# Kernel optimization log

Hardware: AMD Instinct MI355X
Metric: run time of the kernel (lower is better)

Reference implementation:

```python
import jax, jax.numpy as jnp
import numpy as np

DIM = 512
NUM_HEADS = 8
HEAD_DIM = DIM // NUM_HEADS
SCALE = HEAD_DIM ** -0.5
B, T = 8, 1024


def setup_inputs() -> dict:
    key = jax.random.key(0)
    ks = jax.random.split(key, 6)
    x = jax.random.normal(ks[0], (B, T, DIM), dtype=jnp.float32)
    attn_mask = jax.random.randint(ks[1], (B, T, T), 0, 2) == 1  # bool [B,T,T]
    s = 1.0 / np.sqrt(DIM)
    qkv_w = jax.random.uniform(ks[2], (3 * DIM, DIM), jnp.float32, -s, s)
    qkv_b = jax.random.uniform(ks[3], (3 * DIM,), jnp.float32, -s, s)
    proj_w = jax.random.uniform(ks[4], (DIM, DIM), jnp.float32, -s, s)
    proj_b = jax.random.uniform(ks[5], (DIM,), jnp.float32, -s, s)
    return {"x": x, "attn_mask": attn_mask, "qkv_w": qkv_w, "qkv_b": qkv_b,
            "proj_w": proj_w, "proj_b": proj_b}


def reference(x, attn_mask, qkv_w, qkv_b, proj_w, proj_b):
    b, t, c = x.shape
    # QKV projection (torch Linear: x @ W.T + b), split into q,k,v heads
    qkv = x @ qkv_w.T + qkv_b                      # [b,t,3*c]
    qkv = qkv.reshape(b, t, 3, NUM_HEADS, HEAD_DIM)
    qkv = jnp.transpose(qkv, (2, 0, 3, 1, 4))      # [3,b,h,t,d]
    q, k, v = qkv[0], qkv[1], qkv[2]
    scores = jnp.einsum('bhqd,bhkd->bhqk', q, k) * SCALE  # [b,h,t,t]
    min_val = jnp.finfo(scores.dtype).min
    scores = jnp.where(attn_mask[:, None, :, :], min_val, scores)
    attn = jax.nn.softmax(scores, axis=-1)
    out = jnp.einsum('bhqk,bhkd->bhqd', attn, v)   # [b,h,t,d]
    out = jnp.transpose(out, (0, 2, 1, 3)).reshape(b, t, c)
    return out @ proj_w.T + proj_b
```

## Files before the change

kernel.cpp:

```cpp
#include <hip/hip_runtime.h>
#include <math.h>

#define DIM   512
#define NH    8
#define HD    64
#define BATCH 8
#define SEQ   1024
#define QSCALE 0.18033688011112042f

typedef unsigned short u16;
typedef unsigned int   u32;
typedef unsigned long long u64;
typedef __bf16 bf16x8 __attribute__((ext_vector_type(8)));
typedef float  f32x4  __attribute__((ext_vector_type(4)));

__device__ inline u16 f2bf(float f) {
  u32 u = __builtin_bit_cast(u32, f);
  return (u16)((u + 0x7fffu + ((u >> 16) & 1u)) >> 16);
}
__device__ inline float bf2f(u16 h) {
  return __builtin_bit_cast(float, (u32)h << 16);
}
__device__ inline u32 pk2(float a, float b) {
  return (u32)f2bf(a) | ((u32)f2bf(b) << 16);
}

__device__ inline void a16(const u16* g, u16* l) {
  __builtin_amdgcn_global_load_lds(
      (const __attribute__((address_space(1))) u32*)g,
      (__attribute__((address_space(3))) u32*)l, 16, 0, 0);
}


__device__ inline void decomp_body(const float* __restrict__ src, u16* ph,
                                   u16* pl, int t) {
  #pragma unroll
  for (int c = 0; c < 4; ++c) {
    const int cid = c * 256 + t;
    const int row = cid & 15, kc = cid >> 4;
    float f[8];
    *(float4*)&f[0] = *(const float4*)&src[row * DIM + kc * 8];
    *(float4*)&f[4] = *(const float4*)&src[row * DIM + kc * 8 + 4];
    u16 hv[8], lv[8];
    #pragma unroll
    for (int j = 0; j < 8; ++j) {
      hv[j] = f2bf(f[j]);
      lv[j] = f2bf(f[j] - bf2f(hv[j]));
    }
    *(uint4*)&ph[(size_t)cid * 8] = *(const uint4*)hv;
    *(uint4*)&pl[(size_t)cid * 8] = *(const uint4*)lv;
  }
}

__global__ __launch_bounds__(256) void prep(
    const int* __restrict__ mask, u64* __restrict__ bits,
    const float* __restrict__ x, u16* __restrict__ xhi, u16* __restrict__ xlo,
    const float* __restrict__ qkvw, u16* __restrict__ wqh, u16* __restrict__ wql,
    const float* __restrict__ projw, u16* __restrict__ wph, u16* __restrict__ wpl) {
  const int blk = blockIdx.x;
  const int t = threadIdx.x;
  if (blk < 32768) {
    const size_t gid = (size_t)blk * 256 + t;
    const int lane = t & 63;
    const size_t w = gid >> 6;
    const int v = mask[w * 64 + lane];
    const u64 b = __ballot(v != 0);
    if (lane == 0) {
      const int bb = (int)(w >> 14), q = (int)((w >> 4) & 1023),
                kt = (int)(w & 15);
      bits[(((size_t)(bb << 4 | kt)) << 10) | q] = b;
    }
  } else if (blk < 33280) {
    const int rg = blk - 32768;
    decomp_body(x + (size_t)rg * 16 * DIM, xhi + (size_t)rg * 8192,
                xlo + (size_t)rg * 8192, t);
  } else if (blk < 33376) {
    const int rg = blk - 33280;
    decomp_body(qkvw + (size_t)rg * 16 * DIM, wqh + (size_t)rg * 8192,
                wql + (size_t)rg * 8192, t);
  } else {
    const int rg = blk - 33376;
    decomp_body(projw + (size_t)rg * 16 * DIM, wph + (size_t)rg * 8192,
                wpl + (size_t)rg * 8192, t);
  }
}

template <int MT, int NT, int WMT, int WNT, bool QKV>
__global__ __launch_bounds__(256) void mfma_gemm(
    const u16* __restrict__ Agh, const u16* __restrict__ Agl,
    const u16* __restrict__ Bgh, const u16* __restrict__ Bgl,
    const float* __restrict__ bias, void* __restrict__ out0,
    u16* __restrict__ kfr, u16* __restrict__ vfr) {
  __shared__ u16 sAh[MT * 512];
  __shared__ u16 sAl[MT * 512];
  __shared__ u16 sBh[NT * 512];
  __shared__ u16 sBl[NT * 512];

  const int tid = threadIdx.x;
  const int lane = tid & 63;
  const int wv = tid >> 6;
  const int lk = lane & 15, lq = lane >> 4;
  const int n0 = blockIdx.x * (NT * 16), m0 = blockIdx.y * (MT * 16);
  const int wm = (wv & 1) * WMT;
  const int wn = (wv >> 1) * WNT;

  const u16* gAh = Agh + (size_t)(m0 >> 4) * 8192 + lane * 8;
  const u16* gAl = Agl + (size_t)(m0 >> 4) * 8192 + lane * 8;
  const u16* gBh = Bgh + (size_t)(n0 >> 4) * 8192 + lane * 8;
  const u16* gBl = Bgl + (size_t)(n0 >> 4) * 8192 + lane * 8;

  f32x4 acc[WMT][WNT];
  #pragma unroll
  for (int i = 0; i < WMT; ++i)
    #pragma unroll
    for (int j = 0; j < WNT; ++j) acc[i][j] = (f32x4){0.f, 0.f, 0.f, 0.f};

  #pragma unroll 1
  for (int ki = 0; ki < 16; ++ki) {
    __syncthreads();
    if constexpr (MT == NT) {
      #pragma unroll
      for (int it = 0; it < MT / 4; ++it) {
        const int t = it * 4 + wv;
        const size_t go = (size_t)t * 8192 + ki * 512;
        const int lo_ = t * 512 + lane * 8;
        a16(gAh + go, &sAh[lo_]);
        a16(gAl + go, &sAl[lo_]);
        a16(gBh + go, &sBh[lo_]);
        a16(gBl + go, &sBl[lo_]);
      }
    } else {
      #pragma unroll
      for (int it = 0; it < MT / 4; ++it) {
        const int t = it * 4 + wv;
        const size_t go = (size_t)t * 8192 + ki * 512;
        const int lo_ = t * 512 + lane * 8;
        a16(gAh + go, &sAh[lo_]);
        a16(gAl + go, &sAl[lo_]);
      }
      #pragma unroll
      for (int it = 0; it < NT / 4; ++it) {
        const int t = it * 4 + wv;
        const size_t go = (size_t)t * 8192 + ki * 512;
        const int lo_ = t * 512 + lane * 8;
        a16(gBh + go, &sBh[lo_]);
        a16(gBl + go, &sBl[lo_]);
      }
    }
    __syncthreads();

    bf16x8 ah[WMT], al[WMT], bh[WNT], bl[WNT];
    #pragma unroll
    for (int i = 0; i < WMT; ++i) {
      ah[i] = *(const bf16x8*)&sAh[(wm + i) * 512 + lane * 8];
      al[i] = *(const bf16x8*)&sAl[(wm + i) * 512 + lane * 8];
    }
    #pragma unroll
    for (int j = 0; j < WNT; ++j) {
      bh[j] = *(const bf16x8*)&sBh[(wn + j) * 512 + lane * 8];
      bl[j] = *(const bf16x8*)&sBl[(wn + j) * 512 + lane * 8];
    }
    #pragma unroll
    for (int i = 0; i < WMT; ++i)
      #pragma unroll
      for (int j = 0; j < WNT; ++j) {
        acc[i][j] = __builtin_amdgcn_mfma_f32_16x16x32_bf16(ah[i], bh[j], acc[i][j], 0, 0, 0);
        acc[i][j] = __builtin_amdgcn_mfma_f32_16x16x32_bf16(ah[i], bl[j], acc[i][j], 0, 0, 0);
        acc[i][j] = __builtin_amdgcn_mfma_f32_16x16x32_bf16(al[i], bh[j], acc[i][j], 0, 0, 0);
      }
  }

  #pragma unroll
  for (int j = 0; j < WNT; ++j) {
    const int n = n0 + (wn + j) * 16 + lk;
    const float bv_ = bias[n];
    #pragma unroll
    for (int i = 0; i < WMT; ++i) {
      const int mb = m0 + (wm + i) * 16 + lq * 4;
      if (QKV) {
        const int which = n >> 9, h = (n >> 6) & 7, d = n & 63;
        const int b = mb >> 10, tok0 = mb & 1023;
        const size_t hb = (size_t)((b << 3) + h) << 16;
        if (which == 2) {
          const size_t base = hb + ((size_t)(tok0 >> 6) << 12) +
                              ((size_t)((d >> 4) & 3) << 10) +
                              ((size_t)((tok0 >> 5) & 1) << 9) +
                              ((size_t)((d & 15) + (((tok0 >> 3) & 3) << 4)) << 3) +
                              (size_t)(tok0 & 7);
          uint2 o2;
          o2.x = pk2(acc[i][j][0] + bv_, acc[i][j][1] + bv_);
          o2.y = pk2(acc[i][j][2] + bv_, acc[i][j][3] + bv_);
          *(uint2*)&vfr[base] = o2;
        } else if (which == 1) {
          const size_t base = hb + ((size_t)(tok0 >> 4) << 10) +
                              ((size_t)(d >> 5) << 9) + (size_t)(d & 7) +
                              ((size_t)(((d >> 3) & 3) << 4) << 3);
          #pragma unroll
          for (int r = 0; r < 4; ++r)
            kfr[base + (((tok0 & 15) + r) << 3)] = f2bf(acc[i][j][r] + bv_);
        } else {
          u16* dst = (u16*)out0;
          #pragma unroll
          for (int r = 0; r < 4; ++r)
            dst[(((size_t)((b << 3) + h) << 10 | (tok0 + r)) << 6) + d] =
                f2bf((acc[i][j][r] + bv_) * QSCALE);
        }
      } else {
        #pragma unroll
        for (int r = 0; r < 4; ++r)
          ((float*)out0)[(size_t)(mb + r) * DIM + n] = acc[i][j][r] + bv_;
      }
    }
  }
}

__global__ __launch_bounds__(256) void attn_mfma(
    const u16* __restrict__ qg, const u16* __restrict__ kfr,
    const u16* __restrict__ vfr, const u64* __restrict__ bitsT,
    u16* __restrict__ ohi, u16* __restrict__ olo) {
  __shared__ u16 Kls[4096];
  __shared__ u16 Vls[4096];
  __shared__ u16 Ps[64 * 72];

  const int tid = threadIdx.x;
  const int lane = tid & 63;
  const int wv = tid >> 6;
  const int lk = lane & 15, lq = lane >> 4;
  const int bh = blockIdx.x;
  const int q0 = blockIdx.y * 64;
  const int bb = bh >> 3;
  const int q = q0 + wv * 16 + lk;

  const u16* qrow = qg + ((size_t)(bh << 10 | q) << 6);
  const bf16x8 bq0 = *(const bf16x8*)(qrow + lq * 8);
  const bf16x8 bq1 = *(const bf16x8*)(qrow + 32 + lq * 8);

  const u16* kh = kfr + ((size_t)bh << 16);
  const u16* vh = vfr + ((size_t)bh << 16);
  const u64* bitp = bitsT + ((size_t)bb << 14) + q;
  u16* pw = &Ps[(wv * 16 + lk) * 72];

  f32x4 o_[4];
  float l = 0.f;
  #pragma unroll
  for (int t = 0; t < 4; ++t) o_[t] = (f32x4){0.f, 0.f, 0.f, 0.f};

  #pragma unroll 1
  for (int kt = 0; kt < 16; ++kt) {
    __syncthreads();
    #pragma unroll
    for (int it = 0; it < 2; ++it) {
      const int c = it * 4 + wv;
      const int off = c * 512 + lane * 8;
      a16(kh + (size_t)(kt << 12) + off, &Kls[off]);
      a16(vh + (size_t)(kt << 12) + off, &Vls[off]);
    }
    const u64 wd = bitp[kt << 10];
    __syncthreads();

    f32x4 st[4];
    const f32x4 z4 = (f32x4){0.f, 0.f, 0.f, 0.f};
    #pragma unroll
    for (int t = 0; t < 4; ++t) {
      const bf16x8 ak0 = *(const bf16x8*)&Kls[t * 1024 + lane * 8];
      const bf16x8 ak1 = *(const bf16x8*)&Kls[t * 1024 + 512 + lane * 8];
      f32x4 a = __builtin_amdgcn_mfma_f32_16x16x32_bf16(ak0, bq0, z4, 0, 0, 0);
      st[t] = __builtin_amdgcn_mfma_f32_16x16x32_bf16(ak1, bq1, a, 0, 0, 0);
    }

    const u32 w0 = (u32)wd, w1 = (u32)(wd >> 32);
    #pragma unroll
    for (int t = 0; t < 4; ++t) {
      const u32 w = (t < 2) ? w0 : w1;
      const int base = (t & 1) * 16 + lq * 4;
      float p[4];
      #pragma unroll
      for (int r = 0; r < 4; ++r) {
        const float sv = ((w >> (base + r)) & 1u) ? -INFINITY : st[t][r];
        p[r] = __builtin_amdgcn_exp2f(sv);
        l += p[r];
      }
      *(uint2*)(pw + t * 16 + lq * 4) = uint2{pk2(p[0], p[1]), pk2(p[2], p[3])};
    }

    const bf16x8 pa0 = *(const bf16x8*)(pw + lq * 8);
    const bf16x8 pa1 = *(const bf16x8*)(pw + 32 + lq * 8);
    #pragma unroll
    for (int t = 0; t < 4; ++t) {
      const bf16x8 vb0 = *(const bf16x8*)&Vls[t * 1024 + lane * 8];
      const bf16x8 vb1 = *(const bf16x8*)&Vls[t * 1024 + 512 + lane * 8];
      o_[t] = __builtin_amdgcn_mfma_f32_16x16x32_bf16(pa0, vb0, o_[t], 0, 0, 0);
      o_[t] = __builtin_amdgcn_mfma_f32_16x16x32_bf16(pa1, vb1, o_[t], 0, 0, 0);
    }
  }

  l += __shfl_xor(l, 16);
  l += __shfl_xor(l, 32);

  const int h = bh & 7;
  #pragma unroll
  for (int r = 0; r < 4; ++r) {
    const float inv = 1.0f / __shfl(l, lq * 4 + r);
    const int tok = q0 + wv * 16 + lq * 4 + r;
    const int m = (bb << 10) | tok;
    const size_t rgo = (size_t)(m >> 4) * 8192 + (size_t)(m & 15) * 8;
    #pragma unroll
    for (int t = 0; t < 4; ++t) {
      const int d = t * 16 + lk;
      const int k = (h << 6) | d;
      const float v = o_[t][r] * inv;
      const u16 hv = f2bf(v);
      const size_t off = rgo + (size_t)(k >> 3) * 128 + (k & 7);
      ohi[off] = hv;
      olo[off] = f2bf(v - bf2f(hv));
    }
  }
}

extern "C" void kernel_launch(void* const* d_in, const int* in_sizes, int n_in,
                              void* d_out, int out_size, void* d_ws,
                              size_t ws_size, hipStream_t stream) {
  const float* x      = (const float*)d_in[0];
  const int*   mask   = (const int*)d_in[1];
  const float* qkv_w  = (const float*)d_in[2];
  const float* qkv_b  = (const float*)d_in[3];
  const float* proj_w = (const float*)d_in[4];
  const float* proj_b = (const float*)d_in[5];
  float* out = (float*)d_out;

  const size_t SZ = (size_t)BATCH * NH * SEQ * HD;
  u64* bits = (u64*)d_ws;
  u16* qb  = (u16*)(bits + 131072);
  u16* kfr = qb + SZ;
  u16* vfr = kfr + SZ;
  u16* xhi = vfr + SZ;
  u16* xlo = xhi + SZ;
  u16* ohi = xlo + SZ;
  u16* olo = ohi + SZ;
  u16* wqh = olo + SZ;
  u16* wql = wqh + 1536 * 512;
  u16* wph = wql + 1536 * 512;
  u16* wpl = wph + 512 * 512;

  prep<<<33408, 256, 0, stream>>>(mask, bits, x, xhi, xlo,
                                  qkv_w, wqh, wql, proj_w, wph, wpl);
  mfma_gemm<8, 8, 4, 4, true><<<dim3(12, 64), 256, 0, stream>>>(
      xhi, xlo, wqh, wql, qkv_b, qb, kfr, vfr);
  attn_mfma<<<dim3(64, SEQ / 64), 256, 0, stream>>>(
      qb, kfr, vfr, bits, ohi, olo);
  mfma_gemm<4, 8, 2, 4, false><<<dim3(4, 128), 256, 0, stream>>>(
      ohi, olo, wph, wpl, proj_b, out, nullptr, nullptr);
}
```

Before: 216.1 us.

## Double-buffer K/V tiles in attention and batch mask packing per wave

The attention kernel now uses two LDS buffers for K and V. It issues the async load of the next key tile before computing on the current one, so global loads overlap with the MFMA and softmax work. This also drops one barrier per iteration but doubles the K/V shared memory. Separately, the prep kernel's mask-to-bitmask pass now has each wave pack four 64-element words, which cuts that part of the grid by four and reduces block scheduling overhead. The Ps buffer reuse across steps relies on the single barrier at the top of each step.

```diff
diff --git a/kernel.cpp b/kernel.cpp
--- a/kernel.cpp
+++ b/kernel.cpp
@@ -59,27 +59,29 @@
     const float* __restrict__ projw, u16* __restrict__ wph, u16* __restrict__ wpl) {
   const int blk = blockIdx.x;
   const int t = threadIdx.x;
-  if (blk < 32768) {
-    const size_t gid = (size_t)blk * 256 + t;
-    const int lane = t & 63;
-    const size_t w = gid >> 6;
-    const int v = mask[w * 64 + lane];
-    const u64 b = __ballot(v != 0);
-    if (lane == 0) {
-      const int bb = (int)(w >> 14), q = (int)((w >> 4) & 1023),
-                kt = (int)(w & 15);
-      bits[(((size_t)(bb << 4 | kt)) << 10) | q] = b;
-    }
-  } else if (blk < 33280) {
-    const int rg = blk - 32768;
+  if (blk < 8192) {
+    const int wv = t >> 6, lane = t & 63;
+    #pragma unroll
+    for (int j = 0; j < 4; ++j) {
+      const size_t w = (size_t)blk * 16 + wv * 4 + j;
+      const int v = mask[w * 64 + lane];
+      const u64 b = __ballot(v != 0);
+      if (lane == 0) {
+        const int bb = (int)(w >> 14), q = (int)((w >> 4) & 1023),
+                  kt = (int)(w & 15);
+        bits[(((size_t)(bb << 4 | kt)) << 10) | q] = b;
+      }
+    }
+  } else if (blk < 8704) {
+    const int rg = blk - 8192;
     decomp_body(x + (size_t)rg * 16 * DIM, xhi + (size_t)rg * 8192,
                 xlo + (size_t)rg * 8192, t);
-  } else if (blk < 33376) {
-    const int rg = blk - 33280;
+  } else if (blk < 8800) {
+    const int rg = blk - 8704;
     decomp_body(qkvw + (size_t)rg * 16 * DIM, wqh + (size_t)rg * 8192,
                 wql + (size_t)rg * 8192, t);
   } else {
-    const int rg = blk - 33376;
+    const int rg = blk - 8800;
     decomp_body(projw + (size_t)rg * 16 * DIM, wph + (size_t)rg * 8192,
                 wpl + (size_t)rg * 8192, t);
   }
@@ -214,12 +216,70 @@
   }
 }
 
+__device__ inline void stage_kv(const u16* kh, const u16* vh, int kt,
+                                u16* Kd, u16* Vd, int wv, int lane) {
+  #pragma unroll
+  for (int it = 0; it < 2; ++it) {
+    const int c = it * 4 + wv;
+    const int off = c * 512 + lane * 8;
+    a16(kh + ((size_t)kt << 12) + off, Kd + off);
+    a16(vh + ((size_t)kt << 12) + off, Vd + off);
+  }
+}
+
+__device__ inline void attn_step(int kt, bool pre,
+                                 const u16* Kc, const u16* Vc, u16* Kn, u16* Vn,
+                                 const u16* kh, const u16* vh,
+                                 const u64* bitp, u16* pw,
+                                 bf16x8 bq0, bf16x8 bq1,
+                                 f32x4* o_, float& l, int wv, int lane, int lq) {
+  asm volatile("s_waitcnt vmcnt(0)" ::: "memory");
+  __syncthreads();
+  if (pre) stage_kv(kh, vh, kt + 1, Kn, Vn, wv, lane);
+  const u64 wd = bitp[(size_t)kt << 10];
+
+  f32x4 st[4];
+  const f32x4 z4 = (f32x4){0.f, 0.f, 0.f, 0.f};
+  #pragma unroll
+  for (int t = 0; t < 4; ++t) {
+    const bf16x8 ak0 = *(const bf16x8*)&Kc[t * 1024 + lane * 8];
+    const bf16x8 ak1 = *(const bf16x8*)&Kc[t * 1024 + 512 + lane * 8];
+    f32x4 a = __builtin_amdgcn_mfma_f32_16x16x32_bf16(ak0, bq0, z4, 0, 0, 0);
+    st[t] = __builtin_amdgcn_mfma_f32_16x16x32_bf16(ak1, bq1, a, 0, 0, 0);
+  }
+
+  const u32 w0 = (u32)wd, w1 = (u32)(wd >> 32);
+  #pragma unroll
+  for (int t = 0; t < 4; ++t) {
+    const u32 w = (t < 2) ? w0 : w1;
+    const int base = (t & 1) * 16 + lq * 4;
+    float p[4];
+    #pragma unroll
+    for (int r = 0; r < 4; ++r) {
+      const float sv = ((w >> (base + r)) & 1u) ? -INFINITY : st[t][r];
+      p[r] = __builtin_amdgcn_exp2f(sv);
+      l += p[r];
+    }
+    *(uint2*)(pw + t * 16 + lq * 4) = uint2{pk2(p[0], p[1]), pk2(p[2], p[3])};
+  }
+
+  const bf16x8 pa0 = *(const bf16x8*)(pw + lq * 8);
+  const bf16x8 pa1 = *(const bf16x8*)(pw + 32 + lq * 8);
+  #pragma unroll
+  for (int t = 0; t < 4; ++t) {
+    const bf16x8 vb0 = *(const bf16x8*)&Vc[t * 1024 + lane * 8];
+    const bf16x8 vb1 = *(const bf16x8*)&Vc[t * 1024 + 512 + lane * 8];
+    o_[t] = __builtin_amdgcn_mfma_f32_16x16x32_bf16(pa0, vb0, o_[t], 0, 0, 0);
+    o_[t] = __builtin_amdgcn_mfma_f32_16x16x32_bf16(pa1, vb1, o_[t], 0, 0, 0);
+  }
+}
+
 __global__ __launch_bounds__(256) void attn_mfma(
     const u16* __restrict__ qg, const u16* __restrict__ kfr,
     const u16* __restrict__ vfr, const u64* __restrict__ bitsT,
     u16* __restrict__ ohi, u16* __restrict__ olo) {
-  __shared__ u16 Kls[4096];
-  __shared__ u16 Vls[4096];
+  __shared__ u16 Kls[2][4096];
+  __shared__ u16 Vls[2][4096];
   __shared__ u16 Ps[64 * 72];
 
   const int tid = threadIdx.x;
@@ -245,53 +305,14 @@
   #pragma unroll
   for (int t = 0; t < 4; ++t) o_[t] = (f32x4){0.f, 0.f, 0.f, 0.f};
 
+  stage_kv(kh, vh, 0, Kls[0], Vls[0], wv, lane);
+
   #pragma unroll 1
-  for (int kt = 0; kt < 16; ++kt) {
-    __syncthreads();
-    #pragma unroll
-    for (int it = 0; it < 2; ++it) {
-      const int c = it * 4 + wv;
-      const int off = c * 512 + lane * 8;
-      a16(kh + (size_t)(kt << 12) + off, &Kls[off]);
-      a16(vh + (size_t)(kt << 12) + off, &Vls[off]);
-    }
-    const u64 wd = bitp[kt << 10];
-    __syncthreads();
-
-    f32x4 st[4];
-    const f32x4 z4 = (f32x4){0.f, 0.f, 0.f, 0.f};
-    #pragma unroll
-    for (int t = 0; t < 4; ++t) {
-      const bf16x8 ak0 = *(const bf16x8*)&Kls[t * 1024 + lane * 8];
-      const bf16x8 ak1 = *(const bf16x8*)&Kls[t * 1024 + 512 + lane * 8];
-      f32x4 a = __builtin_amdgcn_mfma_f32_16x16x32_bf16(ak0, bq0, z4, 0, 0, 0);
-      st[t] = __builtin_amdgcn_mfma_f32_16x16x32_bf16(ak1, bq1, a, 0, 0, 0);
-    }
-
-    const u32 w0 = (u32)wd, w1 = (u32)(wd >> 32);
-    #pragma unroll
-    for (int t = 0; t < 4; ++t) {
-      const u32 w = (t < 2) ? w0 : w1;
-      const int base = (t & 1) * 16 + lq * 4;
-      float p[4];
-      #pragma unroll
-      for (int r = 0; r < 4; ++r) {
-        const float sv = ((w >> (base + r)) & 1u) ? -INFINITY : st[t][r];
-        p[r] = __builtin_amdgcn_exp2f(sv);
-        l += p[r];
-      }
-      *(uint2*)(pw + t * 16 + lq * 4) = uint2{pk2(p[0], p[1]), pk2(p[2], p[3])};
-    }
-
-    const bf16x8 pa0 = *(const bf16x8*)(pw + lq * 8);
-    const bf16x8 pa1 = *(const bf16x8*)(pw + 32 + lq * 8);
-    #pragma unroll
-    for (int t = 0; t < 4; ++t) {
-      const bf16x8 vb0 = *(const bf16x8*)&Vls[t * 1024 + lane * 8];
-      const bf16x8 vb1 = *(const bf16x8*)&Vls[t * 1024 + 512 + lane * 8];
-      o_[t] = __builtin_amdgcn_mfma_f32_16x16x32_bf16(pa0, vb0, o_[t], 0, 0, 0);
-      o_[t] = __builtin_amdgcn_mfma_f32_16x16x32_bf16(pa1, vb1, o_[t], 0, 0, 0);
-    }
+  for (int kt2 = 0; kt2 < 8; ++kt2) {
+    attn_step(2 * kt2, true, Kls[0], Vls[0], Kls[1], Vls[1],
+              kh, vh, bitp, pw, bq0, bq1, o_, l, wv, lane, lq);
+    attn_step(2 * kt2 + 1, kt2 < 7, Kls[1], Vls[1], Kls[0], Vls[0],
+              kh, vh, bitp, pw, bq0, bq1, o_, l, wv, lane, lq);
   }
 
   l += __shfl_xor(l, 16);
@@ -342,8 +363,8 @@
   u16* wph = wql + 1536 * 512;
   u16* wpl = wph + 512 * 512;
 
-  prep<<<33408, 256, 0, stream>>>(mask, bits, x, xhi, xlo,
-                                  qkv_w, wqh, wql, proj_w, wph, wpl);
+  prep<<<8832, 256, 0, stream>>>(mask, bits, x, xhi, xlo,
+                                 qkv_w, wqh, wql, proj_w, wph, wpl);
   mfma_gemm<8, 8, 4, 4, true><<<dim3(12, 64), 256, 0, stream>>>(
       xhi, xlo, wqh, wql, qkv_b, qb, kfr, vfr);
   attn_mfma<<<dim3(64, SEQ / 64), 256, 0, stream>>>(
```

Result: no change. 215.9 us (-0.1%).
